# Performance work log

Hardware: AMD Instinct MI355X
Metric: run time of the kernel (lower is better)

## Reference

```python
import jax, jax.numpy as jnp
import numpy as np

SEGMENT_LENGTHS = (2048, 4096, 8192)
DILATION_RATES = (1, 2, 4)
NUM_HEADS = 12
EMBED_DIM = 768
B, N = 2, 8192


def setup_inputs() -> dict:
    key = jax.random.key(0)
    ks = jax.random.split(key, 11)
    E = EMBED_DIM
    return {
        "query": jax.random.normal(ks[0], (B, N, E), jnp.float32),
        "key": jax.random.normal(ks[1], (B, N, E), jnp.float32),
        "value": jax.random.normal(ks[2], (B, N, E), jnp.float32),
        "Wq": jax.random.normal(ks[3], (E, E), jnp.float32) * (E ** -0.5),
        "bq": jax.random.normal(ks[4], (E,), jnp.float32) * 0.02,
        "Wk": jax.random.normal(ks[5], (E, E), jnp.float32) * (E ** -0.5),
        "bk": jax.random.normal(ks[6], (E,), jnp.float32) * 0.02,
        "Wv": jax.random.normal(ks[7], (E, E), jnp.float32) * (E ** -0.5),
        "bv": jax.random.normal(ks[8], (E,), jnp.float32) * 0.02,
        "Wo": jax.random.normal(ks[9], (E, E), jnp.float32) * (E ** -0.5),
        "bo": jax.random.normal(ks[10], (E,), jnp.float32) * 0.02,
    }


def _dilated_attention(q, k, v):
    # q, k, v: [b, n, h, d]
    b, n, h, d = q.shape
    num_groups = len(DILATION_RATES)
    g = h // num_groups  # heads per dilation group
    scale = float(1.0 / np.sqrt(d))  # xformers default softmax scale
    out = jnp.zeros_like(q)
    for i, (r, s) in enumerate(zip(DILATION_RATES, SEGMENT_LENGTHS)):
        off = i % r
        hmin, hmax = i * g, (i + 1) * g
        nseg = n // s
        # gather: [b, nseg, s/r, g, d]
        qg = q.reshape(b, nseg, s, h, d)[:, :, off::r, hmin:hmax, :]
        kg = k.reshape(b, nseg, s, h, d)[:, :, off::r, hmin:hmax, :]
        vg = v.reshape(b, nseg, s, h, d)[:, :, off::r, hmin:hmax, :]
        scores = jnp.einsum("bnqhd,bnkhd->bnhqk", qg, kg) * scale
        attn = jax.nn.softmax(scores, axis=-1)
        x = jnp.einsum("bnhqk,bnkhd->bnqhd", attn, vg)
        out = (
            out.reshape(b, nseg, s, h, d)
            .at[:, :, off::r, hmin:hmax, :]
            .add(x)
            .reshape(b, n, h, d)
        )
    # faithful to original: normalize by sum over the sequence dimension
    return out / jnp.sum(out, axis=1, keepdims=True)


def reference(query, key, value, Wq, bq, Wk, bk, Wv, bv, Wo, bo):
    b, n, e = query.shape
    h = NUM_HEADS
    d = e // h
    q = (query @ Wq.T + bq).reshape(b, n, h, d)
    k = (key @ Wk.T + bk).reshape(b, n, h, d)
    v = (value @ Wv.T + bv).reshape(b, n, h, d)
    x = _dilated_attention(q, k, v)
    x = x.reshape(b, n, e)
    return x @ Wo.T + bo
```

## Files before the change

### kernel.cpp

```cpp
#include <hip/hip_runtime.h>
#include <hip/hip_bf16.h>
#include <cmath>
#include <cstdint>

#define B_ 2
#define N_ 8192
#define H_ 12
#define D_ 64
#define E_ 768
#define M_ (B_*N_)

typedef __attribute__((ext_vector_type(8))) short short8;
typedef __attribute__((ext_vector_type(4))) short short4v;
typedef __attribute__((ext_vector_type(4))) float float4v;

__device__ inline short f2b(float f) {
  union { float f; unsigned u; } x; x.f = f;
  unsigned r = (x.u + 0x7fffu + ((x.u >> 16) & 1u)) >> 16;
  return (short)r;
}
__device__ inline float b2f(short s) {
  union { unsigned u; float f; } x; x.u = ((unsigned)(unsigned short)s) << 16;
  return x.f;
}
__device__ inline void split2(float f, short& h, short& l) {
  h = f2b(f);
  l = f2b(f - b2f(h));
}
__device__ inline unsigned pack_trunc(float a, float b) {
  return (__float_as_uint(b) & 0xffff0000u) | (__float_as_uint(a) >> 16);
}

#define MFMA(a, b, c) __builtin_amdgcn_mfma_f32_16x16x32_bf16((a), (b), (c), 0, 0, 0)

#if __has_builtin(__builtin_amdgcn_mfma_f32_16x16x16_bf16)
#define MFMA16(a, b, c) __builtin_amdgcn_mfma_f32_16x16x16_bf16((a), (b), (c), 0, 0, 0)
#elif __has_builtin(__builtin_amdgcn_mfma_f32_16x16x16bf16_1k)
#define MFMA16(a, b, c) __builtin_amdgcn_mfma_f32_16x16x16bf16_1k((a), (b), (c), 0, 0, 0)
#else
__device__ inline float4v mfma16_asm(short4v a, short4v b, float4v c) {
  float4v d = c;
  asm volatile("v_mfma_f32_16x16x16_bf16 %0, %1, %2, %0"
               : "+v"(d) : "v"(a), "v"(b));
  return d;
}
#define MFMA16(a, b, c) mfma16_asm((a), (b), (c))
#endif

#define GLOAD_LDS16(g, l) \
  __builtin_amdgcn_global_load_lds((const __attribute__((address_space(1))) void*)(g), \
      (__attribute__((address_space(3))) void*)(l), 16, 0, 0)

__global__ __launch_bounds__(256) void split_kernel(const float* __restrict__ src,
    short* __restrict__ hi, short* __restrict__ lo, int count4)
{
  int i = blockIdx.x * 256 + threadIdx.x;
  if (i >= count4) return;
  float4v t = ((const float4v*)src)[i];
  short4v h4, l4; short hh, ll;
  split2(t.x, hh, ll); h4.x = hh; l4.x = ll;
  split2(t.y, hh, ll); h4.y = hh; l4.y = ll;
  split2(t.z, hh, ll); h4.z = hh; l4.z = ll;
  split2(t.w, hh, ll); h4.w = hh; l4.w = ll;
  ((short4v*)hi)[i] = h4;
  ((short4v*)lo)[i] = l4;
}

__global__ __launch_bounds__(256) void split_w4(
    const float* __restrict__ w0, const float* __restrict__ w1,
    const float* __restrict__ w2, const float* __restrict__ w3,
    short* __restrict__ planes)
{
  int which = blockIdx.y;
  const float* src = which == 0 ? w0 : which == 1 ? w1 : which == 2 ? w2 : w3;
  short* hi = planes + (size_t)(2 * which) * (E_ * E_);
  short* lo = planes + (size_t)(2 * which + 1) * (E_ * E_);
  int i = blockIdx.x * 256 + threadIdx.x;
  if (i >= E_ * E_ / 4) return;
  float4v t = ((const float4v*)src)[i];
  short4v h4, l4; short hh, ll;
  split2(t.x, hh, ll); h4.x = hh; l4.x = ll;
  split2(t.y, hh, ll); h4.y = hh; l4.y = ll;
  split2(t.z, hh, ll); h4.z = hh; l4.z = ll;
  split2(t.w, hh, ll); h4.w = hh; l4.w = ll;
  ((short4v*)hi)[i] = h4;
  ((short4v*)lo)[i] = l4;
}

__global__ __launch_bounds__(256) void inv_kernel(const float* __restrict__ sums,
    float* __restrict__ inv)
{
  int i = blockIdx.x * 256 + threadIdx.x;
  if (i < B_ * E_) inv[i] = 1.0f / sums[i];
}

__global__ __launch_bounds__(256) void prep_out(const float* __restrict__ attn,
    const float* __restrict__ inv, short* __restrict__ xnh, short* __restrict__ xnl)
{
  size_t e4 = ((size_t)blockIdx.x * 256 + threadIdx.x) * 4;
  int e = (int)(e4 % E_);
  int b = (int)(e4 / ((size_t)E_ * N_));
  float4v a = *(const float4v*)(attn + e4);
  float4v iv = *(const float4v*)(inv + (size_t)b * E_ + e);
  a *= iv;
  short4v h4, l4; short hh, ll;
  split2(a.x, hh, ll); h4.x = hh; l4.x = ll;
  split2(a.y, hh, ll); h4.y = hh; l4.y = ll;
  split2(a.z, hh, ll); h4.z = hh; l4.z = ll;
  split2(a.w, hh, ll); h4.w = hh; l4.w = ll;
  *(short4v*)&xnh[e4] = h4;
  *(short4v*)&xnl[e4] = l4;
}

template<bool OUT_PAIR>
__global__ __launch_bounds__(256) void gemm_dma(
    const short* __restrict__ Ah, const short* __restrict__ Al,
    const short* __restrict__ Wh, const short* __restrict__ Wl,
    const float* __restrict__ bias, void* __restrict__ OutH, short* __restrict__ OutL,
    float oscale)
{
  __shared__ short Ash[4096], Asl[4096], Wsh[4096], Wsl[4096];
  const int tid = threadIdx.x;
  const int flat = blockIdx.x + blockIdx.y * 6;
  const int nid = (flat & 7) * 96 + (flat >> 3);
  const int m0 = (nid / 6) * 128;
  const int n0 = (nid % 6) * 128;
  const int w = tid >> 6, lane = tid & 63, quad = lane >> 4, l16 = lane & 15;
  const int wr = w >> 1, wc = w & 1;
  const int cq = (l16 >> 1) & 3;
  const int dmarow = lane >> 2;
  const int dmacc = (((lane & 3) ^ ((lane >> 3) & 3))) * 8;

  float4v acc[4][4];
#pragma unroll
  for (int a = 0; a < 4; ++a)
#pragma unroll
    for (int c = 0; c < 4; ++c) acc[a][c] = (float4v)0.0f;

  for (int kt = 0; kt < 24; ++kt) {
    const int k0 = kt * 32;
#pragma unroll
    for (int i = 0; i < 2; ++i) {
      int c = w * 2 + i;
      int ldso = c * 512 + lane * 8;
      size_t ga = (size_t)(m0 + c * 16 + dmarow) * E_ + k0 + dmacc;
      size_t gw = (size_t)(n0 + c * 16 + dmarow) * E_ + k0 + dmacc;
      GLOAD_LDS16(Ah + ga, &Ash[ldso]);
      GLOAD_LDS16(Al + ga, &Asl[ldso]);
      GLOAD_LDS16(Wh + gw, &Wsh[ldso]);
      GLOAD_LDS16(Wl + gw, &Wsl[ldso]);
    }
    __syncthreads();

    short8 afh[4], afl[4], bfh[4], bfl[4];
#pragma unroll
    for (int rt = 0; rt < 4; ++rt) {
      int ao = (wr * 64 + rt * 16 + l16) * 32 + (quad ^ cq) * 8;
      afh[rt] = *(const short8*)&Ash[ao];
      afl[rt] = *(const short8*)&Asl[ao];
      int wo = (wc * 64 + rt * 16 + l16) * 32 + (quad ^ cq) * 8;
      bfh[rt] = *(const short8*)&Wsh[wo];
      bfl[rt] = *(const short8*)&Wsl[wo];
    }
#pragma unroll
    for (int rt = 0; rt < 4; ++rt)
#pragma unroll
      for (int ct = 0; ct < 4; ++ct) {
        float4v a = acc[rt][ct];
        a = MFMA(afh[rt], bfh[ct], a);
        a = MFMA(afh[rt], bfl[ct], a);
        a = MFMA(afl[rt], bfh[ct], a);
        acc[rt][ct] = a;
      }
    __syncthreads();
  }

#pragma unroll
  for (int ct = 0; ct < 4; ++ct) {
    int n = n0 + wc * 64 + ct * 16 + l16;
    float bv = bias[n];
#pragma unroll
    for (int rt = 0; rt < 4; ++rt) {
#pragma unroll
      for (int i = 0; i < 4; ++i) {
        int m = m0 + wr * 64 + rt * 16 + quad * 4 + i;
        float v = (acc[rt][ct][i] + bv) * oscale;
        if constexpr (OUT_PAIR) {
          short hh, ll; split2(v, hh, ll);
          ((short*)OutH)[(size_t)m * E_ + n] = hh;
          OutL[(size_t)m * E_ + n] = ll;
        } else {
          ((float*)OutH)[(size_t)m * E_ + n] = v;
        }
      }
    }
  }
}

__device__ __host__ inline int hoff_of(int g, int hg) {
  return g == 0 ? hg * 8192 : (g == 1 ? 32768 + hg * 4096 : 49152 + hg * 2048);
}

__global__ __launch_bounds__(256) void transpose_v(const short* __restrict__ vh,
    const short* __restrict__ vl, short* __restrict__ vgh, short* __restrict__ vgl)
{
  __shared__ short Lh[64 * 68], Ll[64 * 68];
  int bid = blockIdx.x;
  int b = 0;
  if (bid >= 896) { b = 1; bid -= 896; }
  int g, hg, tile;
  if (bid < 512)      { g = 0; hg = bid >> 7; tile = bid & 127; }
  else if (bid < 768) { g = 1; hg = (bid - 512) >> 6; tile = (bid - 512) & 63; }
  else                { g = 2; hg = (bid - 768) >> 5; tile = (bid - 768) & 31; }
  const int h = g * 4 + hg, r = 1 << g, off = g;
  const int ext = 8192 >> g;
  const int jj0 = tile * 64, seg = jj0 >> 11, j0 = jj0 & 2047;
  const int n0 = seg * (2048 << g) + off + j0 * r;
  const int tid = threadIdx.x;

#pragma unroll
  for (int p = 0; p < 2; ++p) {
    int c = tid + p * 256;
    int jr = c >> 3, c8 = (c & 7) * 8;
    size_t gsrc = ((size_t)(b * N_ + n0 + jr * r) * H_ + h) * D_ + c8;
    *(short8*)&Lh[jr * 68 + c8] = *(const short8*)(vh + gsrc);
    *(short8*)&Ll[jr * 68 + c8] = *(const short8*)(vl + gsrc);
  }
  __syncthreads();
  size_t basebh = ((size_t)b * 57344 + hoff_of(g, hg)) * 64;
#pragma unroll
  for (int p = 0; p < 2; ++p) {
    int c = tid + p * 256;
    int dd = c >> 3, jc = (c & 7) * 8;
    short8 oh, ol;
#pragma unroll
    for (int u = 0; u < 8; ++u) {
      oh[u] = Lh[(jc + u) * 68 + dd];
      ol[u] = Ll[(jc + u) * 68 + dd];
    }
    size_t gdst = basebh + (size_t)dd * ext + jj0 + jc;
    *(short8*)(vgh + gdst) = oh;
    *(short8*)(vgl + gdst) = ol;
  }
}

__global__ __launch_bounds__(256, 3) void attn_kernel(
    const short* __restrict__ qh, const short* __restrict__ ql,
    const short* __restrict__ kh, const short* __restrict__ kl,
    const short* __restrict__ vgh, const short* __restrict__ vgl,
    float* __restrict__ attn_out, float* __restrict__ sums)
{
  __shared__ __align__(16) short Vth[2][64 * 32], Vtl[2][64 * 32];

  int bid = (blockIdx.x & 7) * 112 + (blockIdx.x >> 3);
  int g, t;
  if (bid < 512)      { g = 0; t = bid; }
  else if (bid < 768) { g = 1; t = bid - 512; }
  else                { g = 2; t = bid - 768; }
  const int qtile = t & 15; t >>= 4;
  const int hg = t & 3; t >>= 2;
  const int nseg = 4 >> g;
  const int seg = t & (nseg - 1);
  const int b = t / nseg;
  const int r = 1 << g;
  const int off = g;
  const int h = g * 4 + hg;
  const int segbase = seg * (2048 << g);
  const int ext = 8192 >> g;

  const int tid = threadIdx.x;
  const int w = tid >> 6, lane = tid & 63, quad = lane >> 4, l16 = lane & 15;

  const size_t vbase = ((size_t)b * 57344 + hoff_of(g, hg)) * 64 + (size_t)seg * 2048;

  if (g > 0) {
#pragma unroll
    for (int res0 = 1; res0 < 4; ++res0) {
      if (res0 >= r) break;
      int res = (off + res0) & (r - 1);
      for (int c = 0; c < 8; ++c) {
        int idx = tid + c * 256;
        int jl = idx >> 4, d0 = (idx & 15) * 4;
        int pos = segbase + res + (qtile * 128 + jl) * r;
        *(float4v*)(attn_out + ((size_t)(b * N_ + pos) * H_ + h) * D_ + d0) = (float4v)0.f;
      }
    }
  }

  short8 qfh[2][2], qfl[2][2];
#pragma unroll
  for (int qt = 0; qt < 2; ++qt) {
    int j = qtile * 128 + w * 32 + qt * 16 + l16;
    int pos = segbase + off + j * r;
    size_t base = ((size_t)(b * N_ + pos) * H_ + h) * D_;
#pragma unroll
    for (int ks = 0; ks < 2; ++ks) {
      qfh[qt][ks] = *(const short8*)(qh + base + ks * 32 + quad * 8);
      qfl[qt][ks] = *(const short8*)(ql + base + ks * 32 + quad * 8);
    }
  }

  const int vd = tid >> 2;
  const int vc = tid & 3;
  const int vcc = vc ^ ((vd >> 1) & 3);
  const bool vm0 = (vd & 1) != 0;
  const int vldso = vd * 32 + vc * 8;
  const int vrswz = l16 & 7;
  size_t gbV = vbase + (size_t)vd * ext + vcc * 8;

  size_t kbase = ((size_t)(b * N_ + segbase + off + l16 * r) * H_ + h) * D_ + quad * 8;
  const size_t krstep = (size_t)r * (H_ * D_);

  short8 rvh, rvl;
  short8 kf_h[2][2], kf_l[2][2];
#define LOADV(tt) do { size_t va_ = gbV + (size_t)(tt) * 32; \
    rvh = *(const short8*)(vgh + va_); rvl = *(const short8*)(vgl + va_); } while (0)
#define WRITEV(cc) do { \
    short8 th_ = vm0 ? __builtin_shufflevector(rvh, rvh, 4, 5, 6, 7, 0, 1, 2, 3) : rvh; \
    short8 tl_ = vm0 ? __builtin_shufflevector(rvl, rvl, 4, 5, 6, 7, 0, 1, 2, 3) : rvl; \
    *(short8*)&Vth[cc][vldso] = th_; \
    *(short8*)&Vtl[cc][vldso] = tl_; } while (0)
#define KLOAD(tt) do { \
    size_t ka_ = kbase + (size_t)((tt) * 32) * krstep; \
    size_t kb_ = ka_ + 16 * krstep; \
    kf_h[0][0] = *(const short8*)(kh + ka_); \
    kf_h[0][1] = *(const short8*)(kh + ka_ + 32); \
    kf_l[0][0] = *(const short8*)(kl + ka_); \
    kf_l[0][1] = *(const short8*)(kl + ka_ + 32); \
    kf_h[1][0] = *(const short8*)(kh + kb_); \
    kf_h[1][1] = *(const short8*)(kh + kb_ + 32); \
    kf_l[1][0] = *(const short8*)(kl + kb_); \
    kf_l[1][1] = *(const short8*)(kl + kb_ + 32); \
  } while (0)

  float4v o[4][2];
  float mrow[2], lrow[2];
#pragma unroll
  for (int dt = 0; dt < 4; ++dt)
#pragma unroll
    for (int qt = 0; qt < 2; ++qt) o[dt][qt] = (float4v)0.0f;
  mrow[0] = mrow[1] = -INFINITY;
  lrow[0] = lrow[1] = 0.f;

  LOADV(0);
  WRITEV(0);
  LOADV(1);
  KLOAD(0);
  __syncthreads();
  int cur = 0;

  for (int kt = 0; kt < 64; ++kt) {
    WRITEV(cur ^ 1);
    LOADV((kt + 2) & 63);

    float4v sc[2][2];
    __builtin_amdgcn_s_setprio(1);
#pragma unroll
    for (int kvt = 0; kvt < 2; ++kvt) {
#pragma unroll
      for (int qt = 0; qt < 2; ++qt) {
        float4v a = (float4v)0.0f;
        a = MFMA(kf_h[kvt][0], qfh[qt][0], a); a = MFMA(kf_h[kvt][1], qfh[qt][1], a);
        a = MFMA(kf_h[kvt][0], qfl[qt][0], a); a = MFMA(kf_h[kvt][1], qfl[qt][1], a);
        a = MFMA(kf_l[kvt][0], qfh[qt][0], a); a = MFMA(kf_l[kvt][1], qfh[qt][1], a);
        sc[qt][kvt] = a;
      }
    }
    __builtin_amdgcn_s_setprio(0);

    KLOAD((kt + 1) & 63);

    short4v pfh[2][2], pfl[2][2];
#pragma unroll
    for (int qt = 0; qt < 2; ++qt) {
      float mx = fmaxf(fmaxf(fmaxf(sc[qt][0][0], sc[qt][0][1]),
                             fmaxf(sc[qt][0][2], sc[qt][0][3])),
                       fmaxf(fmaxf(sc[qt][1][0], sc[qt][1][1]),
                             fmaxf(sc[qt][1][2], sc[qt][1][3])));
      mx = fmaxf(mx, __shfl_xor(mx, 16, 64));
      mx = fmaxf(mx, __shfl_xor(mx, 32, 64));
      if (__any(mx > mrow[qt] + 8.0f)) {
        float mnew = fmaxf(mrow[qt], mx);
        float alpha = exp2f(mrow[qt] - mnew);
        mrow[qt] = mnew;
        lrow[qt] *= alpha;
#pragma unroll
        for (int dt = 0; dt < 4; ++dt) o[dt][qt] *= alpha;
      }
      float rs = 0.f;
#pragma unroll
      for (int kvt = 0; kvt < 2; ++kvt) {
        float p0 = exp2f(sc[qt][kvt][0] - mrow[qt]);
        float p1 = exp2f(sc[qt][kvt][1] - mrow[qt]);
        float p2 = exp2f(sc[qt][kvt][2] - mrow[qt]);
        float p3 = exp2f(sc[qt][kvt][3] - mrow[qt]);
        rs += (p0 + p1) + (p2 + p3);
        union { unsigned u[2]; short4v s; } ph, pl;
        ph.u[0] = pack_trunc(p0, p1);
        ph.u[1] = pack_trunc(p2, p3);
        float l0 = p0 - __uint_as_float(__float_as_uint(p0) & 0xffff0000u);
        float l1 = p1 - __uint_as_float(__float_as_uint(p1) & 0xffff0000u);
        float l2 = p2 - __uint_as_float(__float_as_uint(p2) & 0xffff0000u);
        float l3 = p3 - __uint_as_float(__float_as_uint(p3) & 0xffff0000u);
        pl.u[0] = pack_trunc(l0, l1);
        pl.u[1] = pack_trunc(l2, l3);
        pfh[qt][kvt] = ph.s;
        pfl[qt][kvt] = pl.s;
      }
      lrow[qt] += rs;
    }

    __builtin_amdgcn_s_setprio(1);
    {
      const short* Vc_h = Vth[cur];
      const short* Vc_l = Vtl[cur];
#pragma unroll
      for (int dt = 0; dt < 4; ++dt) {
#pragma unroll
        for (int kvt = 0; kvt < 2; ++kvt) {
          const int vo = (dt * 16 + l16) * 32 + ((kvt * 4 + quad) ^ vrswz) * 4;
          short4v vfh = *(const short4v*)&Vc_h[vo];
          short4v vfl = *(const short4v*)&Vc_l[vo];
#pragma unroll
          for (int qt = 0; qt < 2; ++qt) {
            float4v a = o[dt][qt];
            a = MFMA16(vfh, pfh[qt][kvt], a);
            a = MFMA16(vfh, pfl[qt][kvt], a);
            a = MFMA16(vfl, pfh[qt][kvt], a);
            o[dt][qt] = a;
          }
        }
      }
    }
    __builtin_amdgcn_s_setprio(0);

    __syncthreads();
    cur ^= 1;
  }
#undef LOADV
#undef WRITEV
#undef KLOAD

  float4v sacc[4];
#pragma unroll
  for (int dt = 0; dt < 4; ++dt) sacc[dt] = (float4v)0.0f;
#pragma unroll
  for (int qt = 0; qt < 2; ++qt) {
    lrow[qt] += __shfl_xor(lrow[qt], 16, 64);
    lrow[qt] += __shfl_xor(lrow[qt], 32, 64);
    float inv_l = 1.0f / lrow[qt];
    int j = qtile * 128 + w * 32 + qt * 16 + l16;
    int pos = segbase + off + j * r;
    float* dst = attn_out + ((size_t)(b * N_ + pos) * H_ + h) * D_;
#pragma unroll
    for (int dt = 0; dt < 4; ++dt) {
      float4v v = o[dt][qt] * inv_l;
      *(float4v*)(dst + dt * 16 + quad * 4) = v;
      sacc[dt] += v;
    }
  }
#pragma unroll
  for (int dt = 0; dt < 4; ++dt) {
#pragma unroll
    for (int i = 0; i < 4; ++i) {
      float x = sacc[dt][i];
      x += __shfl_xor(x, 1, 64);
      x += __shfl_xor(x, 2, 64);
      x += __shfl_xor(x, 4, 64);
      x += __shfl_xor(x, 8, 64);
      if (l16 == 0)
        atomicAdd(&sums[(size_t)b * E_ + h * D_ + dt * 16 + quad * 4 + i], x);
    }
  }
}

extern "C" void kernel_launch(void* const* d_in, const int* in_sizes, int n_in,
                              void* d_out, int out_size, void* d_ws, size_t ws_size,
                              hipStream_t stream)
{
  const float* query = (const float*)d_in[0];
  const float* key_  = (const float*)d_in[1];
  const float* value = (const float*)d_in[2];
  const float* Wq = (const float*)d_in[3];
  const float* bq = (const float*)d_in[4];
  const float* Wk = (const float*)d_in[5];
  const float* bk = (const float*)d_in[6];
  const float* Wv = (const float*)d_in[7];
  const float* bv = (const float*)d_in[8];
  const float* Wo = (const float*)d_in[9];
  const float* bo = (const float*)d_in[10];

  char* ws = (char*)d_ws;
  const size_t szbf = (size_t)M_ * E_ * 2;
  const size_t szvg = (size_t)2 * 57344 * 64 * 2;
  const size_t szw  = (size_t)E_ * E_ * 2;
  short* qh_ = (short*)(ws);
  short* ql_ = (short*)(ws + 1 * szbf);
  short* kh_ = (short*)(ws + 2 * szbf);
  short* kl_ = (short*)(ws + 3 * szbf);
  short* vh_ = (short*)(ws + 4 * szbf);
  short* vl_ = (short*)(ws + 5 * szbf);
  short* ish = (short*)(ws + 6 * szbf);
  short* isl = (short*)(ws + 7 * szbf);
  short* vgh = (short*)(ws + 6 * szbf);
  short* vgl = (short*)(ws + 6 * szbf + szvg);
  short* wsp = (short*)(ws + 8 * szbf);
  float* sums = (float*)(ws + 8 * szbf + 8 * szw);
  float* attn = (float*)(ws + 4 * szbf);
  float* inv  = (float*)qh_;
  short* xnh = kh_;
  short* xnl = kl_;
  short* wqh = wsp + 0 * (szw / 2), *wql = wsp + 1 * (szw / 2);
  short* wkh = wsp + 2 * (szw / 2), *wkl = wsp + 3 * (szw / 2);
  short* wvh = wsp + 4 * (szw / 2), *wvl = wsp + 5 * (szw / 2);
  short* woh = wsp + 6 * (szw / 2), *wol = wsp + 7 * (szw / 2);

  hipMemsetAsync(sums, 0, (size_t)B_ * E_ * sizeof(float), stream);

  split_w4<<<dim3(576, 4), 256, 0, stream>>>(Wq, Wk, Wv, Wo, wsp);

  const int ac4 = M_ * E_ / 4;
  dim3 gg(6, 128), gb(256);
  const float qscale = 0.18033688f;
  split_kernel<<<12288, 256, 0, stream>>>(query, ish, isl, ac4);
  gemm_dma<true><<<gg, gb, 0, stream>>>(ish, isl, wqh, wql, bq, qh_, ql_, qscale);
  split_kernel<<<12288, 256, 0, stream>>>(key_, ish, isl, ac4);
  gemm_dma<true><<<gg, gb, 0, stream>>>(ish, isl, wkh, wkl, bk, kh_, kl_, 1.0f);
  split_kernel<<<12288, 256, 0, stream>>>(value, ish, isl, ac4);
  gemm_dma<true><<<gg, gb, 0, stream>>>(ish, isl, wvh, wvl, bv, vh_, vl_, 1.0f);

  transpose_v<<<1792, 256, 0, stream>>>(vh_, vl_, vgh, vgl);
  attn_kernel<<<896, 256, 0, stream>>>(qh_, ql_, kh_, kl_, vgh, vgl, attn, sums);
  inv_kernel<<<6, 256, 0, stream>>>(sums, inv);
  prep_out<<<12288, 256, 0, stream>>>(attn, inv, xnh, xnl);
  gemm_dma<false><<<gg, gb, 0, stream>>>(xnh, xnl, woh, wol, bo, d_out, nullptr, 1.0f);
}
```

Measured before the change: 831.2 us.

## Halve attention query tile to 64 rows and double grid for occupancy

The attention kernel now gives each wave one 16-row query sub-tile instead of two, so a block covers 64 query rows and the grid doubles to 1792 blocks. Launch bounds rise from 3 to 5 blocks per CU, which cuts per-thread register use and lets more waves hide latency. The LDS swizzle for the V tile is also reworked (new XOR and swap pattern). In exchange, every block now streams the full K and V for its segment, so global and LDS traffic per query row roughly doubles, and there are twice as many atomic adds into the sums.

```diff
diff --git a/kernel.cpp b/kernel.cpp
--- a/kernel.cpp
+++ b/kernel.cpp
@@ -244,7 +244,7 @@
   }
 }
 
-__global__ __launch_bounds__(256, 3) void attn_kernel(
+__global__ __launch_bounds__(256, 5) void attn_kernel(
     const short* __restrict__ qh, const short* __restrict__ ql,
     const short* __restrict__ kh, const short* __restrict__ kl,
     const short* __restrict__ vgh, const short* __restrict__ vgl,
@@ -252,12 +252,12 @@
 {
   __shared__ __align__(16) short Vth[2][64 * 32], Vtl[2][64 * 32];
 
-  int bid = (blockIdx.x & 7) * 112 + (blockIdx.x >> 3);
+  int bid = (blockIdx.x & 7) * 224 + (blockIdx.x >> 3);
   int g, t;
-  if (bid < 512)      { g = 0; t = bid; }
-  else if (bid < 768) { g = 1; t = bid - 512; }
-  else                { g = 2; t = bid - 768; }
-  const int qtile = t & 15; t >>= 4;
+  if (bid < 1024)      { g = 0; t = bid; }
+  else if (bid < 1536) { g = 1; t = bid - 1024; }
+  else                 { g = 2; t = bid - 1536; }
+  const int qtile = t & 31; t >>= 5;
   const int hg = t & 3; t >>= 2;
   const int nseg = 4 >> g;
   const int seg = t & (nseg - 1);
@@ -278,35 +278,34 @@
     for (int res0 = 1; res0 < 4; ++res0) {
       if (res0 >= r) break;
       int res = (off + res0) & (r - 1);
-      for (int c = 0; c < 8; ++c) {
+      for (int c = 0; c < 4; ++c) {
         int idx = tid + c * 256;
         int jl = idx >> 4, d0 = (idx & 15) * 4;
-        int pos = segbase + res + (qtile * 128 + jl) * r;
+        int pos = segbase + res + (qtile * 64 + jl) * r;
         *(float4v*)(attn_out + ((size_t)(b * N_ + pos) * H_ + h) * D_ + d0) = (float4v)0.f;
       }
     }
   }
 
-  short8 qfh[2][2], qfl[2][2];
-#pragma unroll
-  for (int qt = 0; qt < 2; ++qt) {
-    int j = qtile * 128 + w * 32 + qt * 16 + l16;
+  short8 qfh[2], qfl[2];
+  {
+    int j = qtile * 64 + w * 16 + l16;
     int pos = segbase + off + j * r;
     size_t base = ((size_t)(b * N_ + pos) * H_ + h) * D_;
 #pragma unroll
     for (int ks = 0; ks < 2; ++ks) {
-      qfh[qt][ks] = *(const short8*)(qh + base + ks * 32 + quad * 8);
-      qfl[qt][ks] = *(const short8*)(ql + base + ks * 32 + quad * 8);
+      qfh[ks] = *(const short8*)(qh + base + ks * 32 + quad * 8);
+      qfl[ks] = *(const short8*)(ql + base + ks * 32 + quad * 8);
     }
   }
 
   const int vd = tid >> 2;
   const int vc = tid & 3;
-  const int vcc = vc ^ ((vd >> 1) & 3);
-  const bool vm0 = (vd & 1) != 0;
+  const int vg16 = vc ^ ((vd >> 2) & 3);
+  const bool vswap = ((vd >> 1) & 1) != 0;
   const int vldso = vd * 32 + vc * 8;
-  const int vrswz = l16 & 7;
-  size_t gbV = vbase + (size_t)vd * ext + vcc * 8;
+  const int vm = l16 >> 1;
+  size_t gbV = vbase + (size_t)vd * ext + vg16 * 8;
 
   size_t kbase = ((size_t)(b * N_ + segbase + off + l16 * r) * H_ + h) * D_ + quad * 8;
   const size_t krstep = (size_t)r * (H_ * D_);
@@ -316,8 +315,8 @@
 #define LOADV(tt) do { size_t va_ = gbV + (size_t)(tt) * 32; \
     rvh = *(const short8*)(vgh + va_); rvl = *(const short8*)(vgl + va_); } while (0)
 #define WRITEV(cc) do { \
-    short8 th_ = vm0 ? __builtin_shufflevector(rvh, rvh, 4, 5, 6, 7, 0, 1, 2, 3) : rvh; \
-    short8 tl_ = vm0 ? __builtin_shufflevector(rvl, rvl, 4, 5, 6, 7, 0, 1, 2, 3) : rvl; \
+    short8 th_ = vswap ? __builtin_shufflevector(rvh, rvh, 4, 5, 6, 7, 0, 1, 2, 3) : rvh; \
+    short8 tl_ = vswap ? __builtin_shufflevector(rvl, rvl, 4, 5, 6, 7, 0, 1, 2, 3) : rvl; \
     *(short8*)&Vth[cc][vldso] = th_; \
     *(short8*)&Vtl[cc][vldso] = tl_; } while (0)
 #define KLOAD(tt) do { \
@@ -333,14 +332,10 @@
     kf_l[1][1] = *(const short8*)(kl + kb_ + 32); \
   } while (0)
 
-  float4v o[4][2];
-  float mrow[2], lrow[2];
-#pragma unroll
-  for (int dt = 0; dt < 4; ++dt)
-#pragma unroll
-    for (int qt = 0; qt < 2; ++qt) o[dt][qt] = (float4v)0.0f;
-  mrow[0] = mrow[1] = -INFINITY;
-  lrow[0] = lrow[1] = 0.f;
+  float4v o[4];
+  float mrow = -INFINITY, lrow = 0.f;
+#pragma unroll
+  for (int dt = 0; dt < 4; ++dt) o[dt] = (float4v)0.0f;
 
   LOADV(0);
   WRITEV(0);
@@ -353,47 +348,43 @@
     WRITEV(cur ^ 1);
     LOADV((kt + 2) & 63);
 
-    float4v sc[2][2];
+    float4v sc[2];
     __builtin_amdgcn_s_setprio(1);
 #pragma unroll
     for (int kvt = 0; kvt < 2; ++kvt) {
-#pragma unroll
-      for (int qt = 0; qt < 2; ++qt) {
-        float4v a = (float4v)0.0f;
-        a = MFMA(kf_h[kvt][0], qfh[qt][0], a); a = MFMA(kf_h[kvt][1], qfh[qt][1], a);
-        a = MFMA(kf_h[kvt][0], qfl[qt][0], a); a = MFMA(kf_h[kvt][1], qfl[qt][1], a);
-        a = MFMA(kf_l[kvt][0], qfh[qt][0], a); a = MFMA(kf_l[kvt][1], qfh[qt][1], a);
-        sc[qt][kvt] = a;
-      }
+      float4v a = (float4v)0.0f;
+      a = MFMA(kf_h[kvt][0], qfh[0], a); a = MFMA(kf_h[kvt][1], qfh[1], a);
+      a = MFMA(kf_h[kvt][0], qfl[0], a); a = MFMA(kf_h[kvt][1], qfl[1], a);
+      a = MFMA(kf_l[kvt][0], qfh[0], a); a = MFMA(kf_l[kvt][1], qfh[1], a);
+      sc[kvt] = a;
     }
     __builtin_amdgcn_s_setprio(0);
 
     KLOAD((kt + 1) & 63);
 
-    short4v pfh[2][2], pfl[2][2];
-#pragma unroll
-    for (int qt = 0; qt < 2; ++qt) {
-      float mx = fmaxf(fmaxf(fmaxf(sc[qt][0][0], sc[qt][0][1]),
-                             fmaxf(sc[qt][0][2], sc[qt][0][3])),
-                       fmaxf(fmaxf(sc[qt][1][0], sc[qt][1][1]),
-                             fmaxf(sc[qt][1][2], sc[qt][1][3])));
+    short4v pfh[2], pfl[2];
+    {
+      float mx = fmaxf(fmaxf(fmaxf(sc[0][0], sc[0][1]),
+                             fmaxf(sc[0][2], sc[0][3])),
+                       fmaxf(fmaxf(sc[1][0], sc[1][1]),
+                             fmaxf(sc[1][2], sc[1][3])));
       mx = fmaxf(mx, __shfl_xor(mx, 16, 64));
       mx = fmaxf(mx, __shfl_xor(mx, 32, 64));
-      if (__any(mx > mrow[qt] + 8.0f)) {
-        float mnew = fmaxf(mrow[qt], mx);
-        float alpha = exp2f(mrow[qt] - mnew);
-        mrow[qt] = mnew;
-        lrow[qt] *= alpha;
-#pragma unroll
-        for (int dt = 0; dt < 4; ++dt) o[dt][qt] *= alpha;
+      if (__any(mx > mrow + 8.0f)) {
+        float mnew = fmaxf(mrow, mx);
+        float alpha = exp2f(mrow - mnew);
+        mrow = mnew;
+        lrow *= alpha;
+#pragma unroll
+        for (int dt = 0; dt < 4; ++dt) o[dt] *= alpha;
       }
       float rs = 0.f;
 #pragma unroll
       for (int kvt = 0; kvt < 2; ++kvt) {
-        float p0 = exp2f(sc[qt][kvt][0] - mrow[qt]);
-        float p1 = exp2f(sc[qt][kvt][1] - mrow[qt]);
-        float p2 = exp2f(sc[qt][kvt][2] - mrow[qt]);
-        float p3 = exp2f(sc[qt][kvt][3] - mrow[qt]);
+        float p0 = exp2f(sc[kvt][0] - mrow);
+        float p1 = exp2f(sc[kvt][1] - mrow);
+        float p2 = exp2f(sc[kvt][2] - mrow);
+        float p3 = exp2f(sc[kvt][3] - mrow);
         rs += (p0 + p1) + (p2 + p3);
         union { unsigned u[2]; short4v s; } ph, pl;
         ph.u[0] = pack_trunc(p0, p1);
@@ -404,10 +395,10 @@
         float l3 = p3 - __uint_as_float(__float_as_uint(p3) & 0xffff0000u);
         pl.u[0] = pack_trunc(l0, l1);
         pl.u[1] = pack_trunc(l2, l3);
-        pfh[qt][kvt] = ph.s;
-        pfl[qt][kvt] = pl.s;
+        pfh[kvt] = ph.s;
+        pfl[kvt] = pl.s;
       }
-      lrow[qt] += rs;
+      lrow += rs;
     }
 
     __builtin_amdgcn_s_setprio(1);
@@ -418,17 +409,14 @@
       for (int dt = 0; dt < 4; ++dt) {
 #pragma unroll
         for (int kvt = 0; kvt < 2; ++kvt) {
-          const int vo = (dt * 16 + l16) * 32 + ((kvt * 4 + quad) ^ vrswz) * 4;
+          const int vo = (dt * 16 + l16) * 32 + ((kvt * 4 + quad) ^ vm) * 4;
           short4v vfh = *(const short4v*)&Vc_h[vo];
           short4v vfl = *(const short4v*)&Vc_l[vo];
-#pragma unroll
-          for (int qt = 0; qt < 2; ++qt) {
-            float4v a = o[dt][qt];
-            a = MFMA16(vfh, pfh[qt][kvt], a);
-            a = MFMA16(vfh, pfl[qt][kvt], a);
-            a = MFMA16(vfl, pfh[qt][kvt], a);
-            o[dt][qt] = a;
-          }
+          float4v a = o[dt];
+          a = MFMA16(vfh, pfh[kvt], a);
+          a = MFMA16(vfh, pfl[kvt], a);
+          a = MFMA16(vfl, pfh[kvt], a);
+          o[dt] = a;
         }
       }
     }
@@ -444,17 +432,16 @@
   float4v sacc[4];
 #pragma unroll
   for (int dt = 0; dt < 4; ++dt) sacc[dt] = (float4v)0.0f;
-#pragma unroll
-  for (int qt = 0; qt < 2; ++qt) {
-    lrow[qt] += __shfl_xor(lrow[qt], 16, 64);
-    lrow[qt] += __shfl_xor(lrow[qt], 32, 64);
-    float inv_l = 1.0f / lrow[qt];
-    int j = qtile * 128 + w * 32 + qt * 16 + l16;
+  {
+    lrow += __shfl_xor(lrow, 16, 64);
+    lrow += __shfl_xor(lrow, 32, 64);
+    float inv_l = 1.0f / lrow;
+    int j = qtile * 64 + w * 16 + l16;
     int pos = segbase + off + j * r;
     float* dst = attn_out + ((size_t)(b * N_ + pos) * H_ + h) * D_;
 #pragma unroll
     for (int dt = 0; dt < 4; ++dt) {
-      float4v v = o[dt][qt] * inv_l;
+      float4v v = o[dt] * inv_l;
       *(float4v*)(dst + dt * 16 + quad * 4) = v;
       sacc[dt] += v;
     }
@@ -530,7 +517,7 @@
   gemm_dma<true><<<gg, gb, 0, stream>>>(ish, isl, wvh, wvl, bv, vh_, vl_, 1.0f);
 
   transpose_v<<<1792, 256, 0, stream>>>(vh_, vl_, vgh, vgl);
-  attn_kernel<<<896, 256, 0, stream>>>(qh_, ql_, kh_, kl_, vgh, vgl, attn, sums);
+  attn_kernel<<<1792, 256, 0, stream>>>(qh_, ql_, kh_, kl_, vgh, vgl, attn, sums);
   inv_kernel<<<6, 256, 0, stream>>>(sums, inv);
   prep_out<<<12288, 256, 0, stream>>>(attn, inv, xnh, xnl);
   gemm_dma<false><<<gg, gb, 0, stream>>>(xnh, xnl, woh, wol, bo, d_out, nullptr, 1.0f);
```

After: 1.505 ms. 81.1% more time.
